# Optimization experiments

Measured on AMD Instinct MI355X. Metric: run time of the kernel, lower is better.

## Reference

```python
import jax, jax.numpy as jnp
import numpy as np

N, B, E, H = 16384, 16, 131072, 2
NPG = N // B  # nodes per graph
DIMS = [128, 256, 512]  # in==out channels per GAT layer


def setup_inputs() -> dict:
    key = jax.random.key(0)
    ks = iter(jax.random.split(key, 40))
    inp = {"node_feats": jax.random.normal(next(ks), (N, DIMS[0]), jnp.float32)}
    for l, d in enumerate(DIMS):
        s = 1.0 / np.sqrt(d)
        inp[f"W{l}"] = jax.random.normal(next(ks), (d, H * d), jnp.float32) * s
        inp[f"attnl{l}"] = jax.random.normal(next(ks), (H, d), jnp.float32) * 0.1
        inp[f"attnr{l}"] = jax.random.normal(next(ks), (H, d), jnp.float32) * 0.1
        inp[f"resW{l}"] = jax.random.normal(next(ks), (d, H * d), jnp.float32) * s
        inp[f"gamma{l}"] = jnp.ones((d,), jnp.float32)
        inp[f"beta{l}"] = jnp.zeros((d,), jnp.float32)
        inp[f"alpha{l}"] = jnp.ones((d,), jnp.float32)
    dst = jax.random.randint(next(ks), (E,), 0, N, jnp.int32)
    # source node sampled from the same graph as the destination
    src = (dst // NPG) * NPG + jax.random.randint(next(ks), (E,), 0, NPG, jnp.int32)
    inp["edge_src"] = src
    inp["edge_dst"] = dst
    inp["graph_ids"] = jnp.repeat(jnp.arange(B, dtype=jnp.int32), NPG)
    return inp


def _gat(x, W, al, ar, rW, src, dst, d):
    # x: [N, in]; W,rW: [in, H*d]; al,ar: [H,d]
    h = (x @ W).reshape(N, H, d)
    el = jnp.sum(h * al, -1)  # [N,H]
    er = jnp.sum(h * ar, -1)  # [N,H]
    e = jax.nn.leaky_relu(el[src] + er[dst], 0.2)  # [E,H]
    m = jax.ops.segment_max(e, dst, num_segments=N)
    ex = jnp.exp(e - m[dst])
    a = ex / jax.ops.segment_sum(ex, dst, num_segments=N)[dst]  # edge softmax
    out = jax.ops.segment_sum(h[src] * a[:, :, None], dst, num_segments=N)
    return out + (x @ rW).reshape(N, H, d)  # residual projection


def _gnorm(x, gamma, beta, alpha, eps=1e-5):
    # GraphNorm: (x - alpha*mean) / std * gamma + beta, stats over all nodes/heads
    mean = jnp.mean(x, axis=(0, 1), keepdims=True)
    sh = x - alpha * mean
    var = jnp.mean(sh * sh, axis=(0, 1), keepdims=True)
    return gamma * sh * jax.lax.rsqrt(var + eps) + beta


def reference(node_feats, W0, attnl0, attnr0, resW0, gamma0, beta0, alpha0,
              W1, attnl1, attnr1, resW1, gamma1, beta1, alpha1,
              W2, attnl2, attnr2, resW2, gamma2, beta2, alpha2,
              edge_src, edge_dst, graph_ids):
    params = [(W0, attnl0, attnr0, resW0, gamma0, beta0, alpha0),
              (W1, attnl1, attnr1, resW1, gamma1, beta1, alpha1),
              (W2, attnl2, attnr2, resW2, gamma2, beta2, alpha2)]
    counts = jax.ops.segment_sum(jnp.ones((N,), jnp.float32), graph_ids, num_segments=B)
    x = node_feats
    parts = []
    for l, d in enumerate(DIMS):
        W, al, ar, rW, g, b, a_ = params[l]
        x = _gat(x.reshape(N, -1), W, al, ar, rW, edge_src, edge_dst, d)  # [N,H,d]
        x = _gnorm(x, g, b, a_)
        x = jax.nn.leaky_relu(x, 0.01)
        nm = x.mean(1)  # [N,d] head-mean stored as 'updated_feats'
        parts.append(jax.ops.segment_sum(nm, graph_ids, num_segments=B) / counts[:, None])
    return jax.nn.leaky_relu(jnp.concatenate(parts, -1), 0.01)  # [B, 896]
```

## Files before the change

kernel.cpp:

```cpp
#include <hip/hip_runtime.h>
#include <math.h>

constexpr int NNODES  = 16384;
constexpr int NEDGES  = 131072;
constexpr int NGRAPHS = 16;

typedef short bf16x8 __attribute__((ext_vector_type(8)));
typedef short bf16x4 __attribute__((ext_vector_type(4)));
typedef float f32x4  __attribute__((ext_vector_type(4)));

__device__ __forceinline__ float leaky(float x, float s){ return x >= 0.0f ? x : s * x; }

__device__ __forceinline__ unsigned short f2bf(float f){
  unsigned u = __builtin_bit_cast(unsigned, f);
  u += 0x7FFFu + ((u >> 16) & 1u);
  return (unsigned short)(u >> 16);
}
__device__ __forceinline__ float bf2f(unsigned short u){
  unsigned x = (unsigned)u << 16; return __builtin_bit_cast(float, x);
}

__device__ __forceinline__ void gload_lds16(const unsigned short* g, unsigned short* l){
  __builtin_amdgcn_global_load_lds((const __attribute__((address_space(1))) void*)g,
                                   (__attribute__((address_space(3))) void*)l, 16, 0, 0);
}

__global__ void k_deg(const int* __restrict__ dst, int* __restrict__ deg){
  int e = blockIdx.x * 256 + threadIdx.x;
  if (e < NEDGES) atomicAdd(&deg[dst[e]], 1);
}

__global__ __launch_bounds__(1024) void k_scan(const int* __restrict__ deg,
                                               int* __restrict__ rowptr,
                                               int* __restrict__ cursor){
  __shared__ int sums[1024];
  int t = threadIdx.x;
  int loc[16];
  int s = 0;
  #pragma unroll
  for (int i = 0; i < 16; i++){ loc[i] = deg[t*16 + i]; s += loc[i]; }
  sums[t] = s; __syncthreads();
  for (int off = 1; off < 1024; off <<= 1){
    int v = (t >= off) ? sums[t - off] : 0;
    __syncthreads();
    sums[t] += v;
    __syncthreads();
  }
  int base = (t > 0) ? sums[t-1] : 0;
  #pragma unroll
  for (int i = 0; i < 16; i++){
    rowptr[t*16 + i] = base; cursor[t*16 + i] = base; base += loc[i];
  }
  if (t == 1023) rowptr[NNODES] = base;
}

__global__ void k_scatter(const int* __restrict__ src, const int* __restrict__ dst,
                          int* __restrict__ cursor, int* __restrict__ perm){
  int e = blockIdx.x * 256 + threadIdx.x;
  if (e < NEDGES){ int p = atomicAdd(&cursor[dst[e]], 1); perm[p] = src[e]; }
}

__global__ __launch_bounds__(256) void k_counts(const int* __restrict__ gid, float* __restrict__ counts){
  __shared__ int h[NGRAPHS];
  int t = threadIdx.x;
  if (t < NGRAPHS) h[t] = 0;
  __syncthreads();
  int base = blockIdx.x * 1024;
  #pragma unroll
  for (int i = 0; i < 4; i++)
    atomicAdd(&h[gid[base + t + i*256]], 1);
  __syncthreads();
  if (t < NGRAPHS && h[t] > 0) atomicAdd(&counts[t], (float)h[t]);
}

__global__ void k_cvt(const float* __restrict__ in, unsigned short* __restrict__ out, int n4){
  int i = blockIdx.x * 256 + threadIdx.x;
  if (i >= n4) return;
  float4 v = ((const float4*)in)[i];
  ushort4 o; o.x = f2bf(v.x); o.y = f2bf(v.y); o.z = f2bf(v.z); o.w = f2bf(v.w);
  ((ushort4*)out)[i] = o;
}

__global__ __launch_bounds__(256) void k_cvt_t2(const float* __restrict__ W,
                                                const float* __restrict__ RW,
                                                unsigned short* __restrict__ Wt,
                                                unsigned short* __restrict__ RWt,
                                                int K, int NN){
  __shared__ float tile[32][33];
  const float* src = blockIdx.z ? RW : W;
  unsigned short* dst = blockIdx.z ? RWt : Wt;
  int n0 = blockIdx.x * 32, k0 = blockIdx.y * 32;
  int tx = threadIdx.x & 31, ty = threadIdx.x >> 5;
  #pragma unroll
  for (int i = 0; i < 4; i++)
    tile[ty + i*8][tx] = src[(size_t)(k0 + ty + i*8) * NN + n0 + tx];
  __syncthreads();
  #pragma unroll
  for (int i = 0; i < 4; i++)
    dst[(size_t)(n0 + ty + i*8) * K + k0 + tx] = f2bf(tile[tx][ty + i*8]);
}

__global__ __launch_bounds__(256) void k_gemm2(const unsigned short* __restrict__ A,
                                               const unsigned short* __restrict__ Wt,
                                               const unsigned short* __restrict__ RWt,
                                               unsigned short* __restrict__ HB,
                                               unsigned short* __restrict__ RB,
                                               const float* __restrict__ al,
                                               const float* __restrict__ ar,
                                               float* __restrict__ elp,
                                               float* __restrict__ erp,
                                               int K, int NN){
  __shared__ unsigned short As[2][128 * 32];
  __shared__ unsigned short Bs[2][128 * 32];
  int t = threadIdx.x;
  int lane = t & 63, w = t >> 6;
  int nx  = gridDim.x;
  int nwg = nx * gridDim.y;
  int bid = blockIdx.x + blockIdx.y * nx;
  int wg  = (bid & 7) * (nwg >> 3) + (bid >> 3);
  int bx = wg % nx, by = wg / nx;
  int half = nx >> 1;
  bool isW = bx < half;
  const unsigned short* Bt = isW ? Wt : RWt;
  int colB = (isW ? bx : bx - half) * 128;
  int rowA = by * 128;

  int wr = (w >> 1) * 64, wc = (w & 1) * 64;
  int l16 = lane & 15, lhi = lane >> 4;
  f32x4 acc[4][4] = {};

  int srow = t >> 2;
  int skb  = ((t & 3) << 4) ^ (((srow >> 1) & 3) << 4);
  const unsigned short* Ap = A  + (size_t)(rowA + srow) * K + (skb >> 1);
  const unsigned short* Bp = Bt + (size_t)(colB + srow) * K + (skb >> 1);
  size_t rstep = (size_t)64 * K;

  int nt = K >> 5;
  gload_lds16(Ap,         &As[0][t * 8]);
  gload_lds16(Ap + rstep, &As[0][(t + 256) * 8]);
  gload_lds16(Bp,         &Bs[0][t * 8]);
  gload_lds16(Bp + rstep, &Bs[0][(t + 256) * 8]);
  __syncthreads();

  int cur = 0;
  for (int tI = 0; tI < nt; tI++){
    if (tI + 1 < nt){
      int k0n = (tI + 1) << 5;
      gload_lds16(Ap + k0n,         &As[cur ^ 1][t * 8]);
      gload_lds16(Ap + k0n + rstep, &As[cur ^ 1][(t + 256) * 8]);
      gload_lds16(Bp + k0n,         &Bs[cur ^ 1][t * 8]);
      gload_lds16(Bp + k0n + rstep, &Bs[cur ^ 1][(t + 256) * 8]);
    }
    int kb = lhi * 16;
    bf16x8 af[4], bfr[4];
    #pragma unroll
    for (int mi = 0; mi < 4; mi++){
      int row = wr + mi * 16 + l16;
      int off = row * 64 + (kb ^ (((row >> 1) & 3) << 4));
      af[mi] = *(const bf16x8*)((const char*)As[cur] + off);
    }
    #pragma unroll
    for (int ni = 0; ni < 4; ni++){
      int row = wc + ni * 16 + l16;
      int off = row * 64 + (kb ^ (((row >> 1) & 3) << 4));
      bfr[ni] = *(const bf16x8*)((const char*)Bs[cur] + off);
    }
    #pragma unroll
    for (int mi = 0; mi < 4; mi++)
      #pragma unroll
      for (int ni = 0; ni < 4; ni++)
        acc[mi][ni] = __builtin_amdgcn_mfma_f32_16x16x32_bf16(af[mi], bfr[ni], acc[mi][ni], 0, 0, 0);
    __syncthreads();
    cur ^= 1;
  }

  unsigned short* C = isW ? HB : RB;
  #pragma unroll
  for (int mi = 0; mi < 4; mi++){
    #pragma unroll
    for (int j = 0; j < 4; j++){
      int r = rowA + wr + mi * 16 + lhi * 4 + j;
      unsigned short* Cp = C + (size_t)r * NN + colB + wc + l16;
      #pragma unroll
      for (int ni = 0; ni < 4; ni++)
        Cp[ni * 16] = f2bf(acc[mi][ni][j]);
    }
  }

  if (isW){
    int G = NN >> 6;
    int g64 = (colB + wc) >> 6;
    float alv[4], arv[4];
    #pragma unroll
    for (int ni = 0; ni < 4; ni++){
      int col = colB + wc + ni * 16 + l16;
      alv[ni] = al[col]; arv[ni] = ar[col];
    }
    #pragma unroll
    for (int mi = 0; mi < 4; mi++){
      #pragma unroll
      for (int j = 0; j < 4; j++){
        float pe = acc[mi][0][j]*alv[0] + acc[mi][1][j]*alv[1]
                 + acc[mi][2][j]*alv[2] + acc[mi][3][j]*alv[3];
        float pr = acc[mi][0][j]*arv[0] + acc[mi][1][j]*arv[1]
                 + acc[mi][2][j]*arv[2] + acc[mi][3][j]*arv[3];
        #pragma unroll
        for (int o = 8; o; o >>= 1){ pe += __shfl_xor(pe, o); pr += __shfl_xor(pr, o); }
        if (l16 == 0){
          int r = rowA + wr + mi * 16 + lhi * 4 + j;
          elp[(size_t)r * G + g64] = pe;
          erp[(size_t)r * G + g64] = pr;
        }
      }
    }
  }
}

__global__ void k_elred(const float* __restrict__ elp, const float* __restrict__ erp,
                        float* __restrict__ el, float* __restrict__ er, int G){
  int row = blockIdx.x * 256 + threadIdx.x;
  int half = G >> 1;
  float s0 = 0.f, s1 = 0.f, q0 = 0.f, q1 = 0.f;
  const float* ep = elp + (size_t)row * G;
  const float* rp = erp + (size_t)row * G;
  for (int i = 0; i < half; i++){ s0 += ep[i]; q0 += rp[i]; }
  for (int i = half; i < G; i++){ s1 += ep[i]; q1 += rp[i]; }
  el[row*2] = s0; el[row*2+1] = s1;
  er[row*2] = q0; er[row*2+1] = q1;
}

template<int D>
__global__ __launch_bounds__(256) void k_attn(const unsigned short* __restrict__ HB,
                                              unsigned short* __restrict__ RB,
                                              const float* __restrict__ el,
                                              const float* __restrict__ er,
                                              const int* __restrict__ rowptr,
                                              const int* __restrict__ perm){
  constexpr int ITER = (2*D)/256;
  int wid = threadIdx.x >> 6, lane = threadIdx.x & 63;
  int nb = (blockIdx.x & 7) * (NNODES/4/8) + (blockIdx.x >> 3);
  int n = nb * 4 + wid;
  int r0 = rowptr[n], r1 = rowptr[n+1];
  if (r0 == r1) return;
  float er0 = er[n*2], er1 = er[n*2+1];
  float mx0 = -1e30f, mx1 = -1e30f;
  for (int e = r0 + lane; e < r1; e += 64){
    int s = perm[e];
    mx0 = fmaxf(mx0, leaky(el[s*2]   + er0, 0.2f));
    mx1 = fmaxf(mx1, leaky(el[s*2+1] + er1, 0.2f));
  }
  #pragma unroll
  for (int o = 32; o; o >>= 1){ mx0 = fmaxf(mx0, __shfl_xor(mx0, o)); mx1 = fmaxf(mx1, __shfl_xor(mx1, o)); }
  float sm0 = 0.0f, sm1 = 0.0f;
  for (int e = r0 + lane; e < r1; e += 64){
    int s = perm[e];
    sm0 += expf(leaky(el[s*2]   + er0, 0.2f) - mx0);
    sm1 += expf(leaky(el[s*2+1] + er1, 0.2f) - mx1);
  }
  #pragma unroll
  for (int o = 32; o; o >>= 1){ sm0 += __shfl_xor(sm0, o); sm1 += __shfl_xor(sm1, o); }
  float inv0 = 1.0f / sm0, inv1 = 1.0f / sm1;
  float acc[ITER][4];
  #pragma unroll
  for (int j = 0; j < ITER; j++)
    #pragma unroll
    for (int i = 0; i < 4; i++) acc[j][i] = 0.0f;
  for (int e = r0; e < r1; ++e){
    int s = perm[e];
    float a0 = expf(leaky(el[s*2]   + er0, 0.2f) - mx0) * inv0;
    float a1 = expf(leaky(el[s*2+1] + er1, 0.2f) - mx1) * inv1;
    const unsigned short* hrow = HB + (size_t)s * (2*D);
    #pragma unroll
    for (int j = 0; j < ITER; j++){
      int base = j*256 + lane*4;
      bf16x4 v = *(const bf16x4*)(hrow + base);
      float a = (base < D) ? a0 : a1;
      #pragma unroll
      for (int i = 0; i < 4; i++)
        acc[j][i] += a * bf2f((unsigned short)v[i]);
    }
  }
  unsigned short* rrow = RB + (size_t)n * (2*D);
  #pragma unroll
  for (int j = 0; j < ITER; j++){
    int base = j*256 + lane*4;
    bf16x4 r = *(bf16x4*)(rrow + base);
    ushort4 o;
    o.x = f2bf(bf2f((unsigned short)r[0]) + acc[j][0]);
    o.y = f2bf(bf2f((unsigned short)r[1]) + acc[j][1]);
    o.z = f2bf(bf2f((unsigned short)r[2]) + acc[j][2]);
    o.w = f2bf(bf2f((unsigned short)r[3]) + acc[j][3]);
    *(ushort4*)(rrow + base) = o;
  }
}

__global__ __launch_bounds__(256) void k_stats(const unsigned short* __restrict__ R, int nn,
                                               float* __restrict__ gsum, float* __restrict__ gsq){
  int t = threadIdx.x, lane = t & 63, w = t >> 6;
  int c = blockIdx.y * 256 + lane * 4;
  const unsigned short* base = R + (size_t)(blockIdx.x * 128 + w) * nn + c;
  float4 s = make_float4(0,0,0,0), q = make_float4(0,0,0,0);
  #pragma unroll 4
  for (int i = 0; i < 32; i++){
    bf16x4 bv = *(const bf16x4*)(base + (size_t)(i * 4) * nn);
    float vx = bf2f((unsigned short)bv[0]), vy = bf2f((unsigned short)bv[1]);
    float vz = bf2f((unsigned short)bv[2]), vw = bf2f((unsigned short)bv[3]);
    s.x += vx; s.y += vy; s.z += vz; s.w += vw;
    q.x += vx*vx; q.y += vy*vy; q.z += vz*vz; q.w += vw*vw;
  }
  __shared__ float4 rs[256], rq[256];
  rs[t] = s; rq[t] = q; __syncthreads();
  if (t < 64){
    float4 a = rs[t], b = rs[t+64], c2 = rs[t+128], d2 = rs[t+192];
    float4 e = rq[t], f = rq[t+64], g2 = rq[t+128], h2 = rq[t+192];
    int cc = blockIdx.y * 256 + t * 4;
    atomicAdd(&gsum[cc+0], a.x+b.x+c2.x+d2.x);
    atomicAdd(&gsum[cc+1], a.y+b.y+c2.y+d2.y);
    atomicAdd(&gsum[cc+2], a.z+b.z+c2.z+d2.z);
    atomicAdd(&gsum[cc+3], a.w+b.w+c2.w+d2.w);
    atomicAdd(&gsq [cc+0], e.x+f.x+g2.x+h2.x);
    atomicAdd(&gsq [cc+1], e.y+f.y+g2.y+h2.y);
    atomicAdd(&gsq [cc+2], e.z+f.z+g2.z+h2.z);
    atomicAdd(&gsq [cc+3], e.w+f.w+g2.w+h2.w);
  }
}

__global__ __launch_bounds__(256) void k_norm_pool(const unsigned short* __restrict__ R,
                                                   unsigned short* __restrict__ Xn,
                                                   const float* __restrict__ gsum,
                                                   const float* __restrict__ gsq,
                                                   const float* __restrict__ gamma,
                                                   const float* __restrict__ beta,
                                                   const float* __restrict__ alpha,
                                                   float* __restrict__ pool, int d, int loff){
  int t = threadIdx.x, lane = t & 63, w = t >> 6;
  int c = blockIdx.y * 256 + lane * 4;
  int cm = c & (d - 1);
  int nodeb = blockIdx.x * 128;
  int g = blockIdx.x >> 3;
  int nn = 2 * d;
  const float Minv = 1.0f / (2.0f * (float)NNODES);
  float4 gg = *(const float4*)(gamma + cm);
  float4 bb = *(const float4*)(beta + cm);
  float4 aa = *(const float4*)(alpha + cm);
  float mmv[4], rrv[4];
  #pragma unroll
  for (int i = 0; i < 4; i++){
    float m = (gsum[cm+i] + gsum[cm+i+d]) * Minv;
    float q = (gsq [cm+i] + gsq [cm+i+d]) * Minv;
    float a = (i==0)?aa.x:(i==1)?aa.y:(i==2)?aa.z:aa.w;
    float var = q - a * m * m * (2.0f - a);
    mmv[i] = m; rrv[i] = rsqrtf(var + 1e-5f);
  }
  float am0 = aa.x*mmv[0], am1 = aa.y*mmv[1], am2 = aa.z*mmv[2], am3 = aa.w*mmv[3];
  const unsigned short* base = R + (size_t)(nodeb + w) * nn + c;
  unsigned short* xb = Xn ? (Xn + (size_t)(nodeb + w) * nn + c) : nullptr;
  float4 accp = make_float4(0,0,0,0);
  #pragma unroll 4
  for (int i = 0; i < 32; i++){
    bf16x4 bv = *(const bf16x4*)(base + (size_t)(i * 4) * nn);
    float vx = bf2f((unsigned short)bv[0]), vy = bf2f((unsigned short)bv[1]);
    float vz = bf2f((unsigned short)bv[2]), vw = bf2f((unsigned short)bv[3]);
    float y0 = gg.x*(vx-am0)*rrv[0] + bb.x; y0 = y0 >= 0.f ? y0 : 0.01f*y0;
    float y1 = gg.y*(vy-am1)*rrv[1] + bb.y; y1 = y1 >= 0.f ? y1 : 0.01f*y1;
    float y2 = gg.z*(vz-am2)*rrv[2] + bb.z; y2 = y2 >= 0.f ? y2 : 0.01f*y2;
    float y3 = gg.w*(vw-am3)*rrv[3] + bb.w; y3 = y3 >= 0.f ? y3 : 0.01f*y3;
    if (xb){
      ushort4 o; o.x = f2bf(y0); o.y = f2bf(y1); o.z = f2bf(y2); o.w = f2bf(y3);
      *(ushort4*)(xb + (size_t)(i * 4) * nn) = o;
    }
    accp.x += y0; accp.y += y1; accp.z += y2; accp.w += y3;
  }
  __shared__ float4 red[256];
  red[t] = accp; __syncthreads();
  if (t < 64){
    float4 a = red[t], b = red[t+64], c2 = red[t+128], d2 = red[t+192];
    int cc = blockIdx.y * 256 + t * 4;
    float* pb = pool + g * 896 + loff;
    atomicAdd(&pb[(cc+0) & (d-1)], 0.5f*(a.x+b.x+c2.x+d2.x));
    atomicAdd(&pb[(cc+1) & (d-1)], 0.5f*(a.y+b.y+c2.y+d2.y));
    atomicAdd(&pb[(cc+2) & (d-1)], 0.5f*(a.z+b.z+c2.z+d2.z));
    atomicAdd(&pb[(cc+3) & (d-1)], 0.5f*(a.w+b.w+c2.w+d2.w));
  }
}

__global__ void k_final(const float* __restrict__ pool, const float* __restrict__ counts,
                        float* __restrict__ out){
  int idx = blockIdx.x * 256 + threadIdx.x;
  if (idx >= NGRAPHS * 896) return;
  int g = idx / 896;
  float v = pool[idx] / counts[g];
  out[idx] = v >= 0.0f ? v : 0.01f * v;
}

extern "C" void kernel_launch(void* const* d_in, const int* in_sizes, int n_in,
                              void* d_out, int out_size, void* d_ws, size_t ws_size,
                              hipStream_t stream){
  const float* x0 = (const float*)d_in[0];
  const float *W[3], *AL[3], *AR[3], *RW[3], *GA[3], *BE[3], *ALP[3];
  for (int l = 0; l < 3; l++){
    const int b = 1 + l*7;
    W[l]  = (const float*)d_in[b+0];
    AL[l] = (const float*)d_in[b+1];
    AR[l] = (const float*)d_in[b+2];
    RW[l] = (const float*)d_in[b+3];
    GA[l] = (const float*)d_in[b+4];
    BE[l] = (const float*)d_in[b+5];
    ALP[l]= (const float*)d_in[b+6];
  }
  const int* esrc = (const int*)d_in[22];
  const int* edst = (const int*)d_in[23];
  const int* gid  = (const int*)d_in[24];
  float* out = (float*)d_out;

  char* p = (char*)d_ws;
  auto carve = [&](size_t bytes)->void*{
    void* r = (void*)p; p += (bytes + 255) & ~(size_t)255; return r;
  };
  unsigned short* HB = (unsigned short*)carve((size_t)NNODES * 1024 * 2);
  unsigned short* RB = (unsigned short*)carve((size_t)NNODES * 1024 * 2);
  unsigned short* X0b = (unsigned short*)carve((size_t)NNODES * 128 * 2);
  unsigned short* XA  = (unsigned short*)carve((size_t)NNODES * 256 * 2);
  unsigned short* XB  = (unsigned short*)carve((size_t)NNODES * 512 * 2);
  unsigned short* Wt  = (unsigned short*)carve((size_t)1024 * 512 * 2);
  unsigned short* RWt = (unsigned short*)carve((size_t)1024 * 512 * 2);
  float* el     = (float*)carve((size_t)NNODES * 2 * 4);
  float* er     = (float*)carve((size_t)NNODES * 2 * 4);
  float* elp    = (float*)carve((size_t)NNODES * 16 * 4);
  float* erp    = (float*)carve((size_t)NNODES * 16 * 4);
  int*   deg    = (int*)  carve((size_t)NNODES * 4);
  int*   rowptr = (int*)  carve((size_t)(NNODES + 1) * 4);
  int*   cursor = (int*)  carve((size_t)NNODES * 4);
  int*   perm   = (int*)  carve((size_t)NEDGES * 4);
  float* stats  = (float*)carve(3 * 2048 * 4);
  float* pool   = (float*)carve((size_t)NGRAPHS * 896 * 4);
  float* countsF= (float*)carve((size_t)NGRAPHS * 4);
  (void)ws_size; (void)in_sizes; (void)n_in; (void)out_size;

  hipMemsetAsync(deg, 0, NNODES * 4, stream);
  hipMemsetAsync(pool, 0, NGRAPHS * 896 * 4, stream);
  hipMemsetAsync(countsF, 0, NGRAPHS * 4, stream);
  hipMemsetAsync(stats, 0, 3 * 2048 * 4, stream);

  k_deg    <<<NEDGES/256, 256, 0, stream>>>(edst, deg);
  k_scan   <<<1, 1024, 0, stream>>>(deg, rowptr, cursor);
  k_scatter<<<NEDGES/256, 256, 0, stream>>>(esrc, edst, cursor, perm);
  k_counts <<<NNODES/1024, 256, 0, stream>>>(gid, countsF);
  k_cvt    <<<(NNODES*128/4 + 255)/256, 256, 0, stream>>>(x0, X0b, NNODES*128/4);

  const unsigned short* xin = X0b;
  int loff = 0;
  const int dims[3] = {128, 256, 512};
  for (int l = 0; l < 3; l++){
    int d = dims[l], nn = 2*d;
    float* gsum = stats + l * 2048;
    float* gsq  = gsum + 1024;
    dim3 gt(nn/32, d/32, 2);
    k_cvt_t2<<<gt, 256, 0, stream>>>(W[l], RW[l], Wt, RWt, d, nn);
    dim3 gg(2*nn/128, NNODES/128);
    k_gemm2<<<gg, 256, 0, stream>>>(xin, Wt, RWt, HB, RB, AL[l], AR[l], elp, erp, d, nn);
    k_elred<<<NNODES/256, 256, 0, stream>>>(elp, erp, el, er, nn >> 6);
    if (d == 128){
      k_attn<128><<<NNODES/4, 256, 0, stream>>>(HB, RB, el, er, rowptr, perm);
    } else if (d == 256){
      k_attn<256><<<NNODES/4, 256, 0, stream>>>(HB, RB, el, er, rowptr, perm);
    } else {
      k_attn<512><<<NNODES/4, 256, 0, stream>>>(HB, RB, el, er, rowptr, perm);
    }
    dim3 gs(NNODES/128, nn/256);
    k_stats   <<<gs, 256, 0, stream>>>(RB, nn, gsum, gsq);
    unsigned short* xn = (l == 0) ? XA : (l == 1) ? XB : nullptr;
    k_norm_pool<<<gs, 256, 0, stream>>>(RB, xn, gsum, gsq, GA[l], BE[l], ALP[l], pool, d, loff);
    xin = xn; loff += d;
  }
  k_final<<<(NGRAPHS*896 + 255)/256, 256, 0, stream>>>(pool, countsF, out);
}
```

Measured before the change: 339.1 us.

## Overlap GEMM tile loads with explicit vmcnt waits and unroll edge aggregation

```diff
diff --git a/kernel.cpp b/kernel.cpp
--- a/kernel.cpp
+++ b/kernel.cpp
@@ -100,7 +100,7 @@
     dst[(size_t)(n0 + ty + i*8) * K + k0 + tx] = f2bf(tile[tx][ty + i*8]);
 }
 
-__global__ __launch_bounds__(256) void k_gemm2(const unsigned short* __restrict__ A,
+__global__ __launch_bounds__(256, 5) void k_gemm2(const unsigned short* __restrict__ A,
                                                const unsigned short* __restrict__ Wt,
                                                const unsigned short* __restrict__ RWt,
                                                unsigned short* __restrict__ HB,
@@ -140,7 +140,6 @@
   gload_lds16(Ap + rstep, &As[0][(t + 256) * 8]);
   gload_lds16(Bp,         &Bs[0][t * 8]);
   gload_lds16(Bp + rstep, &Bs[0][(t + 256) * 8]);
-  __syncthreads();
 
   int cur = 0;
   for (int tI = 0; tI < nt; tI++){
@@ -150,7 +149,12 @@
       gload_lds16(Ap + k0n + rstep, &As[cur ^ 1][(t + 256) * 8]);
       gload_lds16(Bp + k0n,         &Bs[cur ^ 1][t * 8]);
       gload_lds16(Bp + k0n + rstep, &Bs[cur ^ 1][(t + 256) * 8]);
-    }
+      asm volatile("s_waitcnt vmcnt(4)" ::: "memory");
+    } else {
+      asm volatile("s_waitcnt vmcnt(0)" ::: "memory");
+    }
+    __builtin_amdgcn_s_barrier();
+    __builtin_amdgcn_sched_barrier(0);
     int kb = lhi * 16;
     bf16x8 af[4], bfr[4];
     #pragma unroll
@@ -170,7 +174,7 @@
       #pragma unroll
       for (int ni = 0; ni < 4; ni++)
         acc[mi][ni] = __builtin_amdgcn_mfma_f32_16x16x32_bf16(af[mi], bfr[ni], acc[mi][ni], 0, 0, 0);
-    __syncthreads();
+    __builtin_amdgcn_s_barrier();
     cur ^= 1;
   }
 
@@ -265,7 +269,39 @@
   for (int j = 0; j < ITER; j++)
     #pragma unroll
     for (int i = 0; i < 4; i++) acc[j][i] = 0.0f;
-  for (int e = r0; e < r1; ++e){
+  int e = r0;
+  for (; e + 3 < r1; e += 4){
+    int s0 = perm[e], s1 = perm[e+1], s2 = perm[e+2], s3 = perm[e+3];
+    float w00 = expf(leaky(el[s0*2]   + er0, 0.2f) - mx0) * inv0;
+    float w01 = expf(leaky(el[s0*2+1] + er1, 0.2f) - mx1) * inv1;
+    float w10 = expf(leaky(el[s1*2]   + er0, 0.2f) - mx0) * inv0;
+    float w11 = expf(leaky(el[s1*2+1] + er1, 0.2f) - mx1) * inv1;
+    float w20 = expf(leaky(el[s2*2]   + er0, 0.2f) - mx0) * inv0;
+    float w21 = expf(leaky(el[s2*2+1] + er1, 0.2f) - mx1) * inv1;
+    float w30 = expf(leaky(el[s3*2]   + er0, 0.2f) - mx0) * inv0;
+    float w31 = expf(leaky(el[s3*2+1] + er1, 0.2f) - mx1) * inv1;
+    const unsigned short* h0 = HB + (size_t)s0 * (2*D);
+    const unsigned short* h1 = HB + (size_t)s1 * (2*D);
+    const unsigned short* h2 = HB + (size_t)s2 * (2*D);
+    const unsigned short* h3 = HB + (size_t)s3 * (2*D);
+    #pragma unroll
+    for (int j = 0; j < ITER; j++){
+      int base = j*256 + lane*4;
+      bf16x4 v0 = *(const bf16x4*)(h0 + base);
+      bf16x4 v1 = *(const bf16x4*)(h1 + base);
+      bf16x4 v2 = *(const bf16x4*)(h2 + base);
+      bf16x4 v3 = *(const bf16x4*)(h3 + base);
+      float a0 = (base < D) ? w00 : w01;
+      float a1 = (base < D) ? w10 : w11;
+      float a2 = (base < D) ? w20 : w21;
+      float a3 = (base < D) ? w30 : w31;
+      #pragma unroll
+      for (int i = 0; i < 4; i++)
+        acc[j][i] += a0 * bf2f((unsigned short)v0[i]) + a1 * bf2f((unsigned short)v1[i])
+                   + a2 * bf2f((unsigned short)v2[i]) + a3 * bf2f((unsigned short)v3[i]);
+    }
+  }
+  for (; e < r1; ++e){
     int s = perm[e];
     float a0 = expf(leaky(el[s*2]   + er0, 0.2f) - mx0) * inv0;
     float a1 = expf(leaky(el[s*2+1] + er1, 0.2f) - mx1) * inv1;
```

Result: slower. 364.6 us (+7.5%).
